# Performance work log

Measured on AMD Instinct MI355X. Metric: run time of the kernel, lower is better.

## Reference

```python
import jax, jax.numpy as jnp
import numpy as np

B, H, W, C = 16, 384, 512, 3

def setup_inputs() -> dict:
    key = jax.random.key(0)
    k1, k2, k3 = jax.random.split(key, 3)
    source_img = jax.random.normal(k1, (B, H, W, C), jnp.float32)
    depth_map = jax.random.uniform(k2, (B, H, W), jnp.float32, minval=0.1, maxval=10.0)
    pose = jax.random.normal(k3, (B, 6), jnp.float32)
    intrinsics = jnp.array([[500.0, 0.0, W / 2.0],
                            [0.0, 500.0, H / 2.0],
                            [0.0, 0.0, 1.0]], jnp.float32)
    return {"source_img": source_img, "depth_map": depth_map, "pose": pose,
            "intrinsics": intrinsics}


def _pose_vec2mat(pose):
    # ProjectionLayer scales: translation *= 0.01, rotation (euler rx,ry,rz) *= 0.001
    t = pose[:, :3] * 0.01                       # [B,3]
    r = pose[:, 3:] * 0.001                      # [B,3] euler angles (rx, ry, rz)
    cx, cy, cz = jnp.cos(r[:, 0]), jnp.cos(r[:, 1]), jnp.cos(r[:, 2])
    sx, sy, sz = jnp.sin(r[:, 0]), jnp.sin(r[:, 1]), jnp.sin(r[:, 2])
    z = jnp.zeros_like(cx); o = jnp.ones_like(cx)
    Rz = jnp.stack([cz, -sz, z, sz, cz, z, z, z, o], -1).reshape(-1, 3, 3)
    Ry = jnp.stack([cy, z, sy, z, o, z, -sy, z, cy], -1).reshape(-1, 3, 3)
    Rx = jnp.stack([o, z, z, z, cx, -sx, z, sx, cx], -1).reshape(-1, 3, 3)
    R = Rz @ Ry @ Rx                             # [B,3,3]
    top = jnp.concatenate([R, t[:, :, None]], -1)            # [B,3,4]
    bottom = jnp.broadcast_to(jnp.array([[[0., 0., 0., 1.]]], top.dtype),
                              (top.shape[0], 1, 4))
    return jnp.concatenate([top, bottom], 1)     # [B,4,4]


def _bilinear_sample(img, x, y):
    # img: [B,H,W,C]; x,y: [B,HW] pixel coords. Border-clamped bilinear gather.
    Bn, Hn, Wn, Cn = img.shape
    x0f = jnp.floor(x); y0f = jnp.floor(y)
    x1f = x0f + 1.0;    y1f = y0f + 1.0
    wa = (x1f - x) * (y1f - y)
    wb = (x1f - x) * (y - y0f)
    wc = (x - x0f) * (y1f - y)
    wd = (x - x0f) * (y - y0f)
    x0 = jnp.clip(x0f, 0, Wn - 1).astype(jnp.int32)
    x1 = jnp.clip(x1f, 0, Wn - 1).astype(jnp.int32)
    y0 = jnp.clip(y0f, 0, Hn - 1).astype(jnp.int32)
    y1 = jnp.clip(y1f, 0, Hn - 1).astype(jnp.int32)
    flat = img.reshape(Bn, Hn * Wn, Cn)
    def gather(yi, xi):
        idx = (yi * Wn + xi)[..., None]                      # [B,HW,1]
        return jnp.take_along_axis(flat, idx, axis=1)        # [B,HW,C]
    out = (wa[..., None] * gather(y0, x0) + wb[..., None] * gather(y1, x0)
           + wc[..., None] * gather(y0, x1) + wd[..., None] * gather(y1, x1))
    return out.reshape(Bn, Hn, Wn, Cn)


def reference(source_img, depth_map, pose, intrinsics):
    Bn, Hn, Wn, Cn = source_img.shape
    dt = source_img.dtype
    T = _pose_vec2mat(pose)                                  # [B,4,4] target->source
    Kinv = jnp.linalg.inv(intrinsics)                        # [3,3]
    xs, ys = jnp.meshgrid(jnp.arange(Wn, dtype=dt), jnp.arange(Hn, dtype=dt))
    pix = jnp.stack([xs, ys, jnp.ones_like(xs)], 0).reshape(3, Hn * Wn)  # [3,HW]
    # pixel2cam: depth * K^-1 @ [u,v,1]
    cam = (Kinv @ pix)[None] * depth_map.reshape(Bn, 1, Hn * Wn)         # [B,3,HW]
    cam_h = jnp.concatenate([cam, jnp.ones((Bn, 1, Hn * Wn), dt)], 1)    # [B,4,HW]
    K4 = jnp.zeros((4, 4), dt).at[:3, :3].set(intrinsics).at[3, 3].set(1.0)
    proj = K4[None] @ T                                      # [B,4,4]
    p = proj @ cam_h                                         # [B,4,HW]
    x_src = p[:, 0] / (p[:, 2] + 1e-10)
    y_src = p[:, 1] / (p[:, 2] + 1e-10)
    return _bilinear_sample(source_img, x_src, y_src)        # [B,H,W,C]
```

## Files before the change

kernel.cpp:

```cpp
#include <hip/hip_runtime.h>
#include <math.h>

#define Bn  16
#define Hn  384
#define Wn  512
#define HWn (Hn * Wn)

typedef float f4 __attribute__((ext_vector_type(4)));

__global__ __launch_bounds__(256) void ProjectionLayer_678604833211_kernel(
    const float* __restrict__ src,
    const float* __restrict__ depth,
    const float* __restrict__ pose,
    const float* __restrict__ intr,
    float* __restrict__ out)
{
    __shared__ float S[16];
    __shared__ float rowbuf[4][Wn * 3];

    const int n    = blockIdx.x;
    const int xcd  = n & 7;
    const int m    = n >> 3;
    const int b    = m / 12;
    const int sub  = m - b * 12;
    const int rowblk = xcd * 12 + sub;

    if (threadIdx.x == 0) {
        const float fx = intr[0], cx = intr[2], fy = intr[4], cy = intr[5];
        const float tx = pose[b * 6 + 0] * 0.01f;
        const float ty = pose[b * 6 + 1] * 0.01f;
        const float tz = pose[b * 6 + 2] * 0.01f;
        const float rx = pose[b * 6 + 3] * 0.001f;
        const float ry = pose[b * 6 + 4] * 0.001f;
        const float rz = pose[b * 6 + 5] * 0.001f;
        const float cX = cosf(rx), sX = sinf(rx);
        const float cY = cosf(ry), sY = sinf(ry);
        const float cZ = cosf(rz), sZ = sinf(rz);
        const float R00 = cZ * cY;
        const float R01 = -sZ * cX + cZ * sY * sX;
        const float R02 =  sZ * sX + cZ * sY * cX;
        const float R10 = sZ * cY;
        const float R11 =  cZ * cX + sZ * sY * sX;
        const float R12 = -cZ * sX + sZ * sY * cX;
        const float R20 = -sY;
        const float R21 = cY * sX;
        const float R22 = cY * cX;
        S[0]  = fx * R00 + cx * R20;
        S[1]  = fx * R01 + cx * R21;
        S[2]  = fx * R02 + cx * R22;
        S[3]  = fx * tx  + cx * tz;
        S[4]  = fy * R10 + cy * R20;
        S[5]  = fy * R11 + cy * R21;
        S[6]  = fy * R12 + cy * R22;
        S[7]  = fy * ty  + cy * tz;
        S[8]  = R20;
        S[9]  = R21;
        S[10] = R22;
        S[11] = tz;
        S[12] = 1.0f / fx;
        S[13] = -cx / fx;
        S[14] = 1.0f / fy;
        S[15] = -cy / fy;
    }
    __syncthreads();

    const int wave = threadIdx.x >> 6;
    const int lane = threadIdx.x & 63;
    const int row  = rowblk * 4 + wave;

    const float m0 = S[0],  m1 = S[1],  m2  = S[2],  m3  = S[3];
    const float m4 = S[4],  m5 = S[5],  m6  = S[6],  m7  = S[7];
    const float m8 = S[8],  m9 = S[9],  m10 = S[10], m11 = S[11];
    const float ifx = S[12], nfx = S[13], ify = S[14], nfy = S[15];

    const size_t rowpx = (size_t)b * HWn + (size_t)row * Wn;
    const float* __restrict__ drow = depth + rowpx;

    float dv[8];
    #pragma unroll
    for (int j = 0; j < 8; ++j)
        dv[j] = __builtin_nontemporal_load(drow + j * 64 + lane);

    const float camy_u = fmaf((float)row, ify, nfy);
    const float* __restrict__ base = src + (size_t)b * HWn * 3;
    float* __restrict__ wbuf = &rowbuf[wave][0];

    #pragma unroll
    for (int j = 0; j < 8; ++j) {
        const int   u = j * 64 + lane;
        const float d = dv[j];
        const float camx = fmaf((float)u, ifx, nfx) * d;
        const float camy = camy_u * d;

        const float p0 = fmaf(m0, camx, fmaf(m1, camy, fmaf(m2,  d, m3)));
        const float p1 = fmaf(m4, camx, fmaf(m5, camy, fmaf(m6,  d, m7)));
        const float p2 = fmaf(m8, camx, fmaf(m9, camy, fmaf(m10, d, m11)));

        const float inv = 1.0f / (p2 + 1e-10f);
        const float x = p0 * inv;
        const float y = p1 * inv;

        const float x0f = floorf(x), y0f = floorf(y);
        const float ax = x - x0f;
        const float ay = y - y0f;
        const float bx = (x0f + 1.0f) - x;
        const float by = (y0f + 1.0f) - y;

        const int x0 = (int)fminf(fmaxf(x0f,        0.0f), 511.0f);
        const int x1 = (int)fminf(fmaxf(x0f + 1.0f, 0.0f), 511.0f);
        const int p  = (int)fminf(fmaxf(x0f,        0.0f), 510.0f);
        const int y0 = (int)fminf(fmaxf(y0f,        0.0f), 383.0f);
        const int y1 = (int)fminf(fmaxf(y0f + 1.0f, 0.0f), 383.0f);

        const bool loA = (x0 == p);
        const bool hiC = (x1 == p + 1);
        const float xl = (loA ? bx : 0.0f) + (hiC ? 0.0f : ax);
        const float xh = (loA ? 0.0f : bx) + (hiC ? ax : 0.0f);

        const float* r0 = base + (size_t)(y0 * Wn + p) * 3;
        const float* r1 = base + (size_t)(y1 * Wn + p) * 3;
        float t0[6], t1[6];
        __builtin_memcpy(t0, r0, 24);
        __builtin_memcpy(t1, r1, 24);

        const float o0 = fmaf(by, fmaf(xl, t0[0], xh * t0[3]),
                              ay * fmaf(xl, t1[0], xh * t1[3]));
        const float o1 = fmaf(by, fmaf(xl, t0[1], xh * t0[4]),
                              ay * fmaf(xl, t1[1], xh * t1[4]));
        const float o2 = fmaf(by, fmaf(xl, t0[2], xh * t0[5]),
                              ay * fmaf(xl, t1[2], xh * t1[5]));

        wbuf[u * 3 + 0] = o0;
        wbuf[u * 3 + 1] = o1;
        wbuf[u * 3 + 2] = o2;
    }

    float* __restrict__ orow = out + rowpx * 3;
    #pragma unroll
    for (int k = 0; k < 6; ++k) {
        f4 v = *(const f4*)&wbuf[k * 256 + lane * 4];
        __builtin_nontemporal_store(v, (f4*)(orow + k * 256 + lane * 4));
    }
}

extern "C" void kernel_launch(void* const* d_in, const int* in_sizes, int n_in,
                              void* d_out, int out_size, void* d_ws, size_t ws_size,
                              hipStream_t stream) {
    const float* src   = (const float*)d_in[0];
    const float* depth = (const float*)d_in[1];
    const float* pose  = (const float*)d_in[2];
    const float* intr  = (const float*)d_in[3];
    float* out = (float*)d_out;

    dim3 grid(Bn * 96);
    dim3 block(256);
    ProjectionLayer_678604833211_kernel<<<grid, block, 0, stream>>>(
        src, depth, pose, intr, out);
}
```

Baseline: 108.3 us.

## Use aligned float4 gathers with lane-select shuffles and hoist depth loads above sync

After: 113.8 us. 1.05x slower.

```diff
diff --git a/kernel.cpp b/kernel.cpp
--- a/kernel.cpp
+++ b/kernel.cpp
@@ -24,6 +24,18 @@
     const int b    = m / 12;
     const int sub  = m - b * 12;
     const int rowblk = xcd * 12 + sub;
+
+    const int wave = threadIdx.x >> 6;
+    const int lane = threadIdx.x & 63;
+    const int row  = rowblk * 4 + wave;
+
+    const size_t rowpx = (size_t)b * HWn + (size_t)row * Wn;
+    const float* __restrict__ drow = depth + rowpx;
+
+    float dv[8];
+    #pragma unroll
+    for (int j = 0; j < 8; ++j)
+        dv[j] = drow[j * 64 + lane];
 
     if (threadIdx.x == 0) {
         const float fx = intr[0], cx = intr[2], fy = intr[4], cy = intr[5];
@@ -64,22 +76,10 @@
     }
     __syncthreads();
 
-    const int wave = threadIdx.x >> 6;
-    const int lane = threadIdx.x & 63;
-    const int row  = rowblk * 4 + wave;
-
     const float m0 = S[0],  m1 = S[1],  m2  = S[2],  m3  = S[3];
     const float m4 = S[4],  m5 = S[5],  m6  = S[6],  m7  = S[7];
     const float m8 = S[8],  m9 = S[9],  m10 = S[10], m11 = S[11];
     const float ifx = S[12], nfx = S[13], ify = S[14], nfy = S[15];
-
-    const size_t rowpx = (size_t)b * HWn + (size_t)row * Wn;
-    const float* __restrict__ drow = depth + rowpx;
-
-    float dv[8];
-    #pragma unroll
-    for (int j = 0; j < 8; ++j)
-        dv[j] = __builtin_nontemporal_load(drow + j * 64 + lane);
 
     const float camy_u = fmaf((float)row, ify, nfy);
     const float* __restrict__ base = src + (size_t)b * HWn * 3;
@@ -117,11 +117,49 @@
         const float xl = (loA ? bx : 0.0f) + (hiC ? 0.0f : ax);
         const float xh = (loA ? 0.0f : bx) + (hiC ? ax : 0.0f);
 
-        const float* r0 = base + (size_t)(y0 * Wn + p) * 3;
-        const float* r1 = base + (size_t)(y1 * Wn + p) * 3;
+        const int af0 = (y0 * Wn + p) * 3;
+        const int af1 = (y1 * Wn + p) * 3;
+
+        const f4 qa0 = *(const f4*)(base + (af0 & ~3));
+        const f4 qa1 = *(const f4*)(base + (af0 & ~3) + 4);
+        const float ta5 = base[af0 + 5];
+        const f4 qb0 = *(const f4*)(base + (af1 & ~3));
+        const f4 qb1 = *(const f4*)(base + (af1 & ~3) + 4);
+        const float tb5 = base[af1 + 5];
+
         float t0[6], t1[6];
-        __builtin_memcpy(t0, r0, 24);
-        __builtin_memcpy(t1, r1, 24);
+        {
+            const int k = af0 & 3;
+            const bool k2 = (k & 2) != 0, k1 = (k & 1) != 0;
+            const float A0 = k2 ? qa0.z : qa0.x;
+            const float A1 = k2 ? qa0.w : qa0.y;
+            const float A2 = k2 ? qa1.x : qa0.z;
+            const float A3 = k2 ? qa1.y : qa0.w;
+            const float B0 = k2 ? qa1.z : qa1.x;
+            const float B1 = k2 ? qa1.w : qa1.y;
+            t0[0] = k1 ? A1 : A0;
+            t0[1] = k1 ? A2 : A1;
+            t0[2] = k1 ? A3 : A2;
+            t0[3] = k1 ? B0 : A3;
+            t0[4] = k1 ? B1 : B0;
+            t0[5] = ta5;
+        }
+        {
+            const int k = af1 & 3;
+            const bool k2 = (k & 2) != 0, k1 = (k & 1) != 0;
+            const float A0 = k2 ? qb0.z : qb0.x;
+            const float A1 = k2 ? qb0.w : qb0.y;
+            const float A2 = k2 ? qb1.x : qb0.z;
+            const float A3 = k2 ? qb1.y : qb0.w;
+            const float B0 = k2 ? qb1.z : qb1.x;
+            const float B1 = k2 ? qb1.w : qb1.y;
+            t1[0] = k1 ? A1 : A0;
+            t1[1] = k1 ? A2 : A1;
+            t1[2] = k1 ? A3 : A2;
+            t1[3] = k1 ? B0 : A3;
+            t1[4] = k1 ? B1 : B0;
+            t1[5] = tb5;
+        }
 
         const float o0 = fmaf(by, fmaf(xl, t0[0], xh * t0[3]),
                               ay * fmaf(xl, t1[0], xh * t1[3]));
```

## Convert source image to fp16 in a pre-pass and gather from the half copy

Applied to the files above, without the earlier changes.

New measurement: 105.2 us. -2.9%, faster.

```diff
diff --git a/kernel.cpp b/kernel.cpp
--- a/kernel.cpp
+++ b/kernel.cpp
@@ -1,15 +1,75 @@
 #include <hip/hip_runtime.h>
+#include <hip/hip_fp16.h>
 #include <math.h>
 
 #define Bn  16
 #define Hn  384
 #define Wn  512
 #define HWn (Hn * Wn)
-
-typedef float f4 __attribute__((ext_vector_type(4)));
+#define SRC16_BYTES ((size_t)Bn * HWn * 3 * 2)
+
+typedef float    f4 __attribute__((ext_vector_type(4)));
+typedef unsigned u4 __attribute__((ext_vector_type(4)));
+
+__device__ __forceinline__ unsigned pack2(float a, float b) {
+    __half2 h = __floats2half2_rn(a, b);
+    unsigned r;
+    __builtin_memcpy(&r, &h, 4);
+    return r;
+}
+
+__global__ __launch_bounds__(256) void ProjectionLayer_cvt16_kernel(
+    const float* __restrict__ src, unsigned short* __restrict__ dst)
+{
+    const size_t i = ((size_t)blockIdx.x * 256 + threadIdx.x) * 8;
+    const f4 a = *(const f4*)(src + i);
+    const f4 c = *(const f4*)(src + i + 4);
+    u4 q = {pack2(a.x, a.y), pack2(a.z, a.w), pack2(c.x, c.y), pack2(c.z, c.w)};
+    *(u4*)(dst + i) = q;
+}
+
+__device__ __forceinline__ void setup_S(float* S, const float* pose,
+                                        const float* intr, int b)
+{
+    const float fx = intr[0], cx = intr[2], fy = intr[4], cy = intr[5];
+    const float tx = pose[b * 6 + 0] * 0.01f;
+    const float ty = pose[b * 6 + 1] * 0.01f;
+    const float tz = pose[b * 6 + 2] * 0.01f;
+    const float rx = pose[b * 6 + 3] * 0.001f;
+    const float ry = pose[b * 6 + 4] * 0.001f;
+    const float rz = pose[b * 6 + 5] * 0.001f;
+    const float cX = cosf(rx), sX = sinf(rx);
+    const float cY = cosf(ry), sY = sinf(ry);
+    const float cZ = cosf(rz), sZ = sinf(rz);
+    const float R00 = cZ * cY;
+    const float R01 = -sZ * cX + cZ * sY * sX;
+    const float R02 =  sZ * sX + cZ * sY * cX;
+    const float R10 = sZ * cY;
+    const float R11 =  cZ * cX + sZ * sY * sX;
+    const float R12 = -cZ * sX + sZ * sY * cX;
+    const float R20 = -sY;
+    const float R21 = cY * sX;
+    const float R22 = cY * cX;
+    S[0]  = fx * R00 + cx * R20;
+    S[1]  = fx * R01 + cx * R21;
+    S[2]  = fx * R02 + cx * R22;
+    S[3]  = fx * tx  + cx * tz;
+    S[4]  = fy * R10 + cy * R20;
+    S[5]  = fy * R11 + cy * R21;
+    S[6]  = fy * R12 + cy * R22;
+    S[7]  = fy * ty  + cy * tz;
+    S[8]  = R20;
+    S[9]  = R21;
+    S[10] = R22;
+    S[11] = tz;
+    S[12] = 1.0f / fx;
+    S[13] = -cx / fx;
+    S[14] = 1.0f / fy;
+    S[15] = -cy / fy;
+}
 
 __global__ __launch_bounds__(256) void ProjectionLayer_678604833211_kernel(
-    const float* __restrict__ src,
+    const unsigned* __restrict__ srcu,
     const float* __restrict__ depth,
     const float* __restrict__ pose,
     const float* __restrict__ intr,
@@ -25,64 +85,28 @@
     const int sub  = m - b * 12;
     const int rowblk = xcd * 12 + sub;
 
-    if (threadIdx.x == 0) {
-        const float fx = intr[0], cx = intr[2], fy = intr[4], cy = intr[5];
-        const float tx = pose[b * 6 + 0] * 0.01f;
-        const float ty = pose[b * 6 + 1] * 0.01f;
-        const float tz = pose[b * 6 + 2] * 0.01f;
-        const float rx = pose[b * 6 + 3] * 0.001f;
-        const float ry = pose[b * 6 + 4] * 0.001f;
-        const float rz = pose[b * 6 + 5] * 0.001f;
-        const float cX = cosf(rx), sX = sinf(rx);
-        const float cY = cosf(ry), sY = sinf(ry);
-        const float cZ = cosf(rz), sZ = sinf(rz);
-        const float R00 = cZ * cY;
-        const float R01 = -sZ * cX + cZ * sY * sX;
-        const float R02 =  sZ * sX + cZ * sY * cX;
-        const float R10 = sZ * cY;
-        const float R11 =  cZ * cX + sZ * sY * sX;
-        const float R12 = -cZ * sX + sZ * sY * cX;
-        const float R20 = -sY;
-        const float R21 = cY * sX;
-        const float R22 = cY * cX;
-        S[0]  = fx * R00 + cx * R20;
-        S[1]  = fx * R01 + cx * R21;
-        S[2]  = fx * R02 + cx * R22;
-        S[3]  = fx * tx  + cx * tz;
-        S[4]  = fy * R10 + cy * R20;
-        S[5]  = fy * R11 + cy * R21;
-        S[6]  = fy * R12 + cy * R22;
-        S[7]  = fy * ty  + cy * tz;
-        S[8]  = R20;
-        S[9]  = R21;
-        S[10] = R22;
-        S[11] = tz;
-        S[12] = 1.0f / fx;
-        S[13] = -cx / fx;
-        S[14] = 1.0f / fy;
-        S[15] = -cy / fy;
-    }
-    __syncthreads();
-
     const int wave = threadIdx.x >> 6;
     const int lane = threadIdx.x & 63;
     const int row  = rowblk * 4 + wave;
+
+    const size_t rowpx = (size_t)b * HWn + (size_t)row * Wn;
+    const float* __restrict__ drow = depth + rowpx;
+
+    float dv[8];
+    #pragma unroll
+    for (int j = 0; j < 8; ++j)
+        dv[j] = drow[j * 64 + lane];
+
+    if (threadIdx.x == 0) setup_S(S, pose, intr, b);
+    __syncthreads();
 
     const float m0 = S[0],  m1 = S[1],  m2  = S[2],  m3  = S[3];
     const float m4 = S[4],  m5 = S[5],  m6  = S[6],  m7  = S[7];
     const float m8 = S[8],  m9 = S[9],  m10 = S[10], m11 = S[11];
     const float ifx = S[12], nfx = S[13], ify = S[14], nfy = S[15];
 
-    const size_t rowpx = (size_t)b * HWn + (size_t)row * Wn;
-    const float* __restrict__ drow = depth + rowpx;
-
-    float dv[8];
-    #pragma unroll
-    for (int j = 0; j < 8; ++j)
-        dv[j] = __builtin_nontemporal_load(drow + j * 64 + lane);
-
     const float camy_u = fmaf((float)row, ify, nfy);
-    const float* __restrict__ base = src + (size_t)b * HWn * 3;
+    const unsigned* __restrict__ basep = srcu + (size_t)b * (HWn * 3 / 2);
     float* __restrict__ wbuf = &rowbuf[wave][0];
 
     #pragma unroll
@@ -117,22 +141,130 @@
         const float xl = (loA ? bx : 0.0f) + (hiC ? 0.0f : ax);
         const float xh = (loA ? 0.0f : bx) + (hiC ? ax : 0.0f);
 
-        const float* r0 = base + (size_t)(y0 * Wn + p) * 3;
-        const float* r1 = base + (size_t)(y1 * Wn + p) * 3;
-        float t0[6], t1[6];
-        __builtin_memcpy(t0, r0, 24);
-        __builtin_memcpy(t1, r1, 24);
-
-        const float o0 = fmaf(by, fmaf(xl, t0[0], xh * t0[3]),
-                              ay * fmaf(xl, t1[0], xh * t1[3]));
-        const float o1 = fmaf(by, fmaf(xl, t0[1], xh * t0[4]),
-                              ay * fmaf(xl, t1[1], xh * t1[4]));
-        const float o2 = fmaf(by, fmaf(xl, t0[2], xh * t0[5]),
-                              ay * fmaf(xl, t1[2], xh * t1[5]));
+        const int ci = (3 * p) >> 1;
+        unsigned qa[4], qb[4];
+        __builtin_memcpy(qa, basep + y0 * 768 + ci, 16);
+        __builtin_memcpy(qb, basep + y1 * 768 + ci, 16);
+
+        const bool odd = (p & 1) != 0;
+        unsigned Ea0 = odd ? __builtin_amdgcn_alignbit(qa[1], qa[0], 16) : qa[0];
+        unsigned Ea1 = odd ? __builtin_amdgcn_alignbit(qa[2], qa[1], 16) : qa[1];
+        unsigned Ea2 = odd ? __builtin_amdgcn_alignbit(qa[3], qa[2], 16) : qa[2];
+        unsigned Eb0 = odd ? __builtin_amdgcn_alignbit(qb[1], qb[0], 16) : qb[0];
+        unsigned Eb1 = odd ? __builtin_amdgcn_alignbit(qb[2], qb[1], 16) : qb[1];
+        unsigned Eb2 = odd ? __builtin_amdgcn_alignbit(qb[3], qb[2], 16) : qb[2];
+
+        __half2 ha0, ha1, ha2, hb0, hb1, hb2;
+        __builtin_memcpy(&ha0, &Ea0, 4);
+        __builtin_memcpy(&ha1, &Ea1, 4);
+        __builtin_memcpy(&ha2, &Ea2, 4);
+        __builtin_memcpy(&hb0, &Eb0, 4);
+        __builtin_memcpy(&hb1, &Eb1, 4);
+        __builtin_memcpy(&hb2, &Eb2, 4);
+        const float2 Fa0 = __half22float2(ha0);
+        const float2 Fa1 = __half22float2(ha1);
+        const float2 Fa2 = __half22float2(ha2);
+        const float2 Fb0 = __half22float2(hb0);
+        const float2 Fb1 = __half22float2(hb1);
+        const float2 Fb2 = __half22float2(hb2);
+
+        const float o0 = fmaf(by, fmaf(xl, Fa0.x, xh * Fa1.y),
+                              ay * fmaf(xl, Fb0.x, xh * Fb1.y));
+        const float o1 = fmaf(by, fmaf(xl, Fa0.y, xh * Fa2.x),
+                              ay * fmaf(xl, Fb0.y, xh * Fb2.x));
+        const float o2 = fmaf(by, fmaf(xl, Fa1.x, xh * Fa2.y),
+                              ay * fmaf(xl, Fb1.x, xh * Fb2.y));
 
         wbuf[u * 3 + 0] = o0;
         wbuf[u * 3 + 1] = o1;
         wbuf[u * 3 + 2] = o2;
+    }
+
+    float* __restrict__ orow = out + rowpx * 3;
+    #pragma unroll
+    for (int k = 0; k < 6; ++k) {
+        f4 v = *(const f4*)&wbuf[k * 256 + lane * 4];
+        __builtin_nontemporal_store(v, (f4*)(orow + k * 256 + lane * 4));
+    }
+}
+
+__global__ __launch_bounds__(256) void ProjectionLayer_fp32_kernel(
+    const float* __restrict__ src, const float* __restrict__ depth,
+    const float* __restrict__ pose, const float* __restrict__ intr,
+    float* __restrict__ out)
+{
+    __shared__ float S[16];
+    __shared__ float rowbuf[4][Wn * 3];
+
+    const int n    = blockIdx.x;
+    const int xcd  = n & 7;
+    const int m    = n >> 3;
+    const int b    = m / 12;
+    const int sub  = m - b * 12;
+    const int rowblk = xcd * 12 + sub;
+
+    const int wave = threadIdx.x >> 6;
+    const int lane = threadIdx.x & 63;
+    const int row  = rowblk * 4 + wave;
+
+    const size_t rowpx = (size_t)b * HWn + (size_t)row * Wn;
+    const float* __restrict__ drow = depth + rowpx;
+
+    float dv[8];
+    #pragma unroll
+    for (int j = 0; j < 8; ++j)
+        dv[j] = drow[j * 64 + lane];
+
+    if (threadIdx.x == 0) setup_S(S, pose, intr, b);
+    __syncthreads();
+
+    const float m0 = S[0],  m1 = S[1],  m2  = S[2],  m3  = S[3];
+    const float m4 = S[4],  m5 = S[5],  m6  = S[6],  m7  = S[7];
+    const float m8 = S[8],  m9 = S[9],  m10 = S[10], m11 = S[11];
+    const float ifx = S[12], nfx = S[13], ify = S[14], nfy = S[15];
+
+    const float camy_u = fmaf((float)row, ify, nfy);
+    const float* __restrict__ base = src + (size_t)b * HWn * 3;
+    float* __restrict__ wbuf = &rowbuf[wave][0];
+
+    #pragma unroll
+    for (int j = 0; j < 8; ++j) {
+        const int   u = j * 64 + lane;
+        const float d = dv[j];
+        const float camx = fmaf((float)u, ifx, nfx) * d;
+        const float camy = camy_u * d;
+        const float p0 = fmaf(m0, camx, fmaf(m1, camy, fmaf(m2,  d, m3)));
+        const float p1 = fmaf(m4, camx, fmaf(m5, camy, fmaf(m6,  d, m7)));
+        const float p2 = fmaf(m8, camx, fmaf(m9, camy, fmaf(m10, d, m11)));
+        const float inv = 1.0f / (p2 + 1e-10f);
+        const float x = p0 * inv;
+        const float y = p1 * inv;
+
+        const float x0f = floorf(x), y0f = floorf(y);
+        const float ax = x - x0f, ay = y - y0f;
+        const float bx = (x0f + 1.0f) - x, by = (y0f + 1.0f) - y;
+
+        const int x0 = (int)fminf(fmaxf(x0f,        0.0f), 511.0f);
+        const int x1 = (int)fminf(fmaxf(x0f + 1.0f, 0.0f), 511.0f);
+        const int p  = (int)fminf(fmaxf(x0f,        0.0f), 510.0f);
+        const int y0 = (int)fminf(fmaxf(y0f,        0.0f), 383.0f);
+        const int y1 = (int)fminf(fmaxf(y0f + 1.0f, 0.0f), 383.0f);
+
+        const bool loA = (x0 == p);
+        const bool hiC = (x1 == p + 1);
+        const float xl = (loA ? bx : 0.0f) + (hiC ? 0.0f : ax);
+        const float xh = (loA ? 0.0f : bx) + (hiC ? ax : 0.0f);
+
+        float t0[6], t1[6];
+        __builtin_memcpy(t0, base + (size_t)(y0 * Wn + p) * 3, 24);
+        __builtin_memcpy(t1, base + (size_t)(y1 * Wn + p) * 3, 24);
+
+        wbuf[u * 3 + 0] = fmaf(by, fmaf(xl, t0[0], xh * t0[3]),
+                               ay * fmaf(xl, t1[0], xh * t1[3]));
+        wbuf[u * 3 + 1] = fmaf(by, fmaf(xl, t0[1], xh * t0[4]),
+                               ay * fmaf(xl, t1[1], xh * t1[4]));
+        wbuf[u * 3 + 2] = fmaf(by, fmaf(xl, t0[2], xh * t0[5]),
+                               ay * fmaf(xl, t1[2], xh * t1[5]));
     }
 
     float* __restrict__ orow = out + rowpx * 3;
@@ -152,8 +284,14 @@
     const float* intr  = (const float*)d_in[3];
     float* out = (float*)d_out;
 
-    dim3 grid(Bn * 96);
-    dim3 block(256);
-    ProjectionLayer_678604833211_kernel<<<grid, block, 0, stream>>>(
-        src, depth, pose, intr, out);
-}
+    if (ws_size >= SRC16_BYTES + 16) {
+        unsigned short* src16 = (unsigned short*)d_ws;
+        ProjectionLayer_cvt16_kernel<<<dim3(Bn * HWn * 3 / (256 * 8)), dim3(256),
+                                       0, stream>>>(src, src16);
+        ProjectionLayer_678604833211_kernel<<<dim3(Bn * 96), dim3(256), 0, stream>>>(
+            (const unsigned*)src16, depth, pose, intr, out);
+    } else {
+        ProjectionLayer_fp32_kernel<<<dim3(Bn * 96), dim3(256), 0, stream>>>(
+            src, depth, pose, intr, out);
+    }
+}
```
